# Kernel optimization log

Measured on AMD Instinct MI355X. Metric: run time of the kernel, lower is better.

## Reference

```python
import jax, jax.numpy as jnp
import numpy as np
import math

B, H, L, DK, D, LOCAL = 4, 8, 2048, 64, 512, 4


def setup_inputs() -> dict:
    key = jax.random.key(0)
    ks = jax.random.split(key, 9)
    n = L
    return {
        'query': jax.random.normal(ks[0], (B, H, L, DK), jnp.float32),
        'key': jax.random.normal(ks[1], (B, H, L, DK), jnp.float32),
        'value': jax.random.normal(ks[2], (B, H, L, DK), jnp.float32),
        'users': jax.random.normal(ks[3], (B, L, D), jnp.float32),
        'mask': jnp.tril(jnp.ones((L, L), dtype=bool))[None, None],  # causal [1,1,L,L]
        'rel_pos_w': jax.random.normal(ks[4], (2 * n - 1, DK * LOCAL), jnp.float32) * 0.02,
        'user_proj_w': jax.random.normal(ks[5], (DK * LOCAL, D), jnp.float32) * 0.02,
        'user_proj_b': jax.random.normal(ks[6], (DK * LOCAL,), jnp.float32) * 0.02,
        'mlp_w': jax.random.normal(ks[7], (LOCAL, DK), jnp.float32) * 0.1,
        'mlp_b': jax.random.normal(ks[8], (LOCAL,), jnp.float32) * 0.1,
    }


def reference(query, key, value, users, mask, rel_pos_w, user_proj_w, user_proj_b, mlp_w, mlp_b):
    b, h, l, dk = query.shape
    local = mlp_w.shape[0]
    g = h - local
    n = l
    scale = 1.0 / math.sqrt(dk)
    NEG = -1e12  # MAX_VAL in the torch source

    # ---- global heads: plain softmax attention ----
    qg, kg, vg = query[:, :g], key[:, :g], value[:, :g]
    sg = jnp.einsum('bhqd,bhkd->bhqk', qg, kg) * scale
    sg = jnp.where(mask, sg, NEG)
    pg = jax.nn.softmax(sg, axis=-1)
    og = jnp.einsum('bhqk,bhkd->bhqd', pg, vg)

    # ---- local (LOCKER) heads ----
    ql, kl, vl = query[:, g:], key[:, g:], value[:, g:]
    sl = jnp.einsum('bhqd,bhkd->bhqk', ql, kl) * scale

    # reweight = Linear(d_k,1)(rel_pos + v_q + v_k + user_proj(users)_q) per local head.
    # Linear over a sum decomposes exactly (same math, avoids [b,local,l,l,dk] tensor):
    rel_tab = rel_pos_w.reshape(2 * n - 1, local, dk)
    rel_scores = jnp.einsum('rhd,hd->rh', rel_tab, mlp_w)          # [2n-1, local]
    pos = jnp.arange(n)
    distance = pos[None, :] - pos[:, None] + n - 1                  # [l, l]
    rel_term = rel_scores[distance].transpose(2, 0, 1)              # [local, l, l]

    v_term = jnp.einsum('bhkd,hd->bhk', vl, mlp_w)                  # [b, local, l]
    u = (users @ user_proj_w.T + user_proj_b).reshape(b, l, local, dk)
    u_term = jnp.einsum('bqhd,hd->bhq', u, mlp_w)                   # [b, local, l]

    reweight = (rel_term[None]
                + v_term[:, :, None, :]      # value_l.unsqueeze(-3): varies over key idx
                + v_term[:, :, :, None]      # value_l.unsqueeze(-2): varies over query idx
                + u_term[:, :, :, None]      # user term broadcast over key idx
                + mlp_b[None, :, None, None])

    sl = sl + reweight
    sl = jnp.where(mask, sl, NEG)
    pl = jax.nn.softmax(sl, axis=-1)
    ol = jnp.einsum('bhqk,bhkd->bhqd', pl, vl)

    return jnp.concatenate([og, ol], axis=1)  # [b, h, l, d_k]
```

## Files before the change

kernel.cpp:

```cpp
#include <hip/hip_runtime.h>

#define TL 2048
#define NHEAD 8
#define NLOC 4
#define L2E 1.44269504f
#define PSTRIDE 4352

typedef __attribute__((ext_vector_type(4))) float f32x4;
typedef __attribute__((ext_vector_type(16))) float f32x16;
typedef __attribute__((ext_vector_type(8))) __bf16 bf16x8;
typedef __attribute__((ext_vector_type(8))) unsigned short u16x8;
typedef __attribute__((ext_vector_type(4))) unsigned int u32x4;

static __device__ __forceinline__ unsigned short f2bf(float f) {
    unsigned u = __float_as_uint(f);
    u = (u + 0x7FFFu + ((u >> 16) & 1u)) >> 16;
    return (unsigned short)u;
}
static __device__ __forceinline__ unsigned int cvtpk(float a, float b) {
    unsigned int w;
    asm("v_cvt_pk_bf16_f32 %0, %1, %2" : "=v"(w) : "v"(a), "v"(b));
    return w;
}
static __device__ __forceinline__ void gl_lds16(const void* g, void* l) {
    __builtin_amdgcn_global_load_lds(
        (const __attribute__((address_space(1))) void*)g,
        (__attribute__((address_space(3))) void*)l, 16, 0, 0);
}

__global__ __launch_bounds__(256) void preconv_kernel(
    const float* __restrict__ key, const float* __restrict__ value,
    const float* __restrict__ mlp_w, const float* __restrict__ rel_pos_w,
    unsigned short* __restrict__ Kb, unsigned short* __restrict__ Vtb,
    float* __restrict__ vtbf, float* __restrict__ rel_sf) {
    int blk = blockIdx.x;
    int t = threadIdx.x;
    int wave = t >> 6, lane = t & 63;

    if (blk >= 1024) {
        int r = (blk - 1024) * 4 + wave;
        if (r < 2 * TL - 1) {
#pragma unroll
            for (int hp = 0; hp < 4; ++hp) {
                float v = rel_pos_w[r * 256 + hp * 64 + lane] * mlp_w[hp * 64 + lane];
#pragma unroll
                for (int off = 32; off; off >>= 1) v += __shfl_xor(v, off);
                if (lane == 0) rel_sf[hp * 4096 + r] = v * L2E;
            }
        }
        return;
    }

    __shared__ float Tf[64][66];
    int bh = blk >> 5, kt = blk & 31;
    int h = bh & 7, b = bh >> 3;
    size_t src = (size_t)blk * 4096;
    size_t dst = (size_t)blk * 4096;

    {
        int row = t >> 2, q4 = t & 3;
        const float* kp = key + src + row * 64 + q4 * 16;
#pragma unroll
        for (int j = 0; j < 4; ++j)
            *(f32x4*)&Tf[row][q4 * 16 + j * 4] = *(const f32x4*)(kp + j * 4);
    }
    __syncthreads();
#pragma unroll
    for (int i = 0; i < 2; ++i) {
        int idx = t + i * 256;
        int l31 = idx & 31, hi = (idx >> 5) & 1, mq = (idx >> 6) & 3, h2 = idx >> 8;
        int r = h2 * 32 + l31, c = mq * 2 + hi;
        u16x8 o;
#pragma unroll
        for (int j = 0; j < 8; ++j) o[j] = f2bf(Tf[r][c * 8 + j]);
        *(u16x8*)&Kb[dst + idx * 8] = o;
    }
    __syncthreads();

    {
        int row = t >> 2, q4 = t & 3;
        const float* vp = value + src + row * 64 + q4 * 16;
#pragma unroll
        for (int j = 0; j < 4; ++j)
            *(f32x4*)&Tf[row][q4 * 16 + j * 4] = *(const f32x4*)(vp + j * 4);
    }
    __syncthreads();
#pragma unroll
    for (int i = 0; i < 2; ++i) {
        int idx = t + i * 256;
        int l31 = idx & 31, hi = (idx >> 5) & 1, half = (idx >> 6) & 1, c2 = idx >> 7;
        int r = half * 32 + l31, c = c2 * 2 + hi;
        u16x8 o;
#pragma unroll
        for (int j = 0; j < 8; ++j) o[j] = f2bf(Tf[c * 8 + j][r]);
        *(u16x8*)&Vtb[dst + idx * 8] = o;
    }
    if (h >= NLOC) {
        float mw = mlp_w[(h - NLOC) * 64 + lane];
        float* vout = vtbf + (size_t)((b * NLOC + h - NLOC) * TL) + kt * 64;
#pragma unroll
        for (int i = 0; i < 16; ++i) {
            int row = wave * 16 + i;
            float v = Tf[row][lane] * mw;
#pragma unroll
            for (int off = 32; off; off >>= 1) v += __shfl_xor(v, off);
            if (lane == 0) vout[row] = v * L2E;
        }
    }
}

#define MFMA32(A, B, C) __builtin_amdgcn_mfma_f32_32x32x16_bf16(A, B, C, 0, 0, 0)

__global__ __launch_bounds__(256, 4) void attn_kernel(
    const float* __restrict__ query,
    const unsigned short* __restrict__ Kb, const unsigned short* __restrict__ Vtb,
    const float* __restrict__ rel_sf, const float* __restrict__ vtbf,
    float* __restrict__ part) {

    __shared__ __align__(16) unsigned char smem[35328];
    unsigned short* Ks0 = (unsigned short*)smem;
    unsigned short* Vt0 = (unsigned short*)(smem + 16384);
    float* relw  = (float*)(smem + 32768);
    float* biasf = (float*)(smem + 34816);

    int bid = blockIdx.x;
    int bhx = bid & 31;
    int bh = (bhx & 7) * 4 + (bhx >> 3);
    int sid = bid >> 5;
    int i = 0, s = 0, acc = 0;
    for (int ii = 15; ii >= 0; --ii) {
        int ns = (2 * ii + 7) / 6;
        if (sid >= acc && sid < acc + ns) { i = ii; s = sid - acc; }
        acc += ns;
    }
    int nt = 2 * i + 2;
    int n = (2 * i + 7) / 6;
    int T = nt / n, R = nt % n;
    int k_b = s * T + min(s, R);
    int len = T + (s < R ? 1 : 0);
    int q0 = i << 7;

    int h = bh & 7, b = bh >> 3;
    bool islocal = (h >= NLOC);
    int t = threadIdx.x;
    int w = t >> 6;
    int l31 = t & 31;
    int hi = (t >> 5) & 1;
    int qrel = 32 * w + l31;
    int qglob = q0 + qrel;
    int qmaxw = q0 + 32 * w + 31;
    int hivl = hi * 256 + l31 * 8;

    size_t tbase = (size_t)bh * 32 * 4096;
    const unsigned short* Ktiles = Kb + tbase;
    const unsigned short* Vtiles = Vtb + tbase;
    const float* vtpf = vtbf + (islocal ? (size_t)((b * NLOC + h - NLOC) * TL) : 0);
    int idxlo = 64 * k_b - q0 + 1920;
    const float* relsrc = rel_sf + (islocal ? ((h - NLOC) * 4096 + idxlo) : 0);

    gl_lds16(Ktiles + (size_t)k_b * 4096 + t * 8, Ks0 + t * 8);
    gl_lds16(Ktiles + (size_t)k_b * 4096 + 2048 + t * 8, Ks0 + 2048 + t * 8);
    gl_lds16(Vtiles + (size_t)k_b * 4096 + t * 8, Vt0 + t * 8);
    gl_lds16(Vtiles + (size_t)k_b * 4096 + 2048 + t * 8, Vt0 + 2048 + t * 8);
    if (islocal) {
        if (t < 128) {
            f32x4 v = ((const f32x4*)relsrc)[t];
            ((f32x4*)relw)[t] = v - 20.0f;
        }
        if (t < 16) ((f32x4*)biasf)[t] = ((const f32x4*)(vtpf + (size_t)k_b * 64))[t];
    }

    const float SC = 0.125f * L2E;
    bf16x8 qf[4];
    {
        const float* qsrc = query + ((size_t)bh * TL + qglob) * 64 + 8 * hi;
#pragma unroll
        for (int mq = 0; mq < 4; ++mq) {
            f32x4 a = *(const f32x4*)(qsrc + 16 * mq);
            f32x4 c = *(const f32x4*)(qsrc + 16 * mq + 4);
            u16x8 u;
#pragma unroll
            for (int j = 0; j < 4; ++j) { u[j] = f2bf(a[j] * SC); u[4 + j] = f2bf(c[j] * SC); }
            qf[mq] = __builtin_bit_cast(bf16x8, u);
        }
    }

    float lsum = 0.f;
    f32x16 O0 = {0,0,0,0,0,0,0,0,0,0,0,0,0,0,0,0};
    f32x16 O1 = {0,0,0,0,0,0,0,0,0,0,0,0,0,0,0,0};

    __syncthreads();

    int cur = 0;
#pragma unroll 1
    for (int kt4 = 0; kt4 < len; ++kt4) {
        int kt = k_b + kt4;
        unsigned short* Ks = Ks0 + cur * 4096;
        unsigned short* Vt = Vt0 + cur * 4096;
        const float* bias = biasf + cur * 64;

        if (kt4 + 1 < len) {
            int nb = cur ^ 1;
            const unsigned short* gk = Ktiles + (size_t)(kt + 1) * 4096;
            const unsigned short* gv = Vtiles + (size_t)(kt + 1) * 4096;
            gl_lds16(gk + t * 8, Ks0 + nb * 4096 + t * 8);
            gl_lds16(gk + 2048 + t * 8, Ks0 + nb * 4096 + 2048 + t * 8);
            gl_lds16(gv + t * 8, Vt0 + nb * 4096 + t * 8);
            gl_lds16(gv + 2048 + t * 8, Vt0 + nb * 4096 + 2048 + t * 8);
            if (islocal && t < 16)
                ((f32x4*)(biasf + nb * 64))[t] =
                    ((const f32x4*)(vtpf + (size_t)(kt + 1) * 64))[t];
        }

        bool active = (64 * kt <= qmaxw);
        bool maskt = (64 * kt + 63 > q0 + 32 * w);
        if (active) {
#pragma unroll
            for (int h2 = 0; h2 < 2; ++h2) {
                f32x16 S;
                if (islocal) {
                    int rbase = 64 * kt4 + 32 * h2 + 4 * hi + 127 - qrel;
#pragma unroll
                    for (int g = 0; g < 4; ++g) {
                        f32x4 bv = *(const f32x4*)&bias[32 * h2 + 8 * g + 4 * hi];
#pragma unroll
                        for (int j = 0; j < 4; ++j)
                            S[4 * g + j] = bv[j] + relw[rbase + 8 * g + j];
                    }
                } else {
                    S = (f32x16){-20.f,-20.f,-20.f,-20.f,-20.f,-20.f,-20.f,-20.f,
                                 -20.f,-20.f,-20.f,-20.f,-20.f,-20.f,-20.f,-20.f};
                }
                __builtin_amdgcn_s_setprio(1);
#pragma unroll
                for (int mq = 0; mq < 4; ++mq) {
                    const bf16x8 kf = *(const bf16x8*)&Ks[(h2 * 4 + mq) * 512 + hivl];
                    S = MFMA32(kf, qf[mq], S);
                }
                __builtin_amdgcn_s_setprio(0);

                if (maskt) {
                    int koff = 64 * kt + 32 * h2 + 4 * hi - qglob;
#pragma unroll
                    for (int r = 0; r < 16; ++r) {
                        int kk = (r & 3) + 8 * (r >> 2);
                        if (koff + kk > 0) S[r] = -1e30f;
                    }
                }
                float ps = 0.f;
#pragma unroll
                for (int r = 0; r < 16; ++r) {
                    float p = exp2f(S[r]);
                    S[r] = p; ps += p;
                }
                ps += __shfl_xor(ps, 32);
                lsum += ps;

                __builtin_amdgcn_s_setprio(1);
#pragma unroll
                for (int kq = 0; kq < 2; ++kq) {
                    int ra = 8 * kq;
                    unsigned int x0 = cvtpk(S[ra + 0], S[ra + 1]);
                    unsigned int x1 = cvtpk(S[ra + 2], S[ra + 3]);
                    unsigned int y0 = cvtpk(S[ra + 4], S[ra + 5]);
                    unsigned int y1 = cvtpk(S[ra + 6], S[ra + 7]);
                    asm("v_permlane32_swap_b32 %0, %1" : "+v"(x0), "+v"(y0));
                    asm("v_permlane32_swap_b32 %0, %1" : "+v"(x1), "+v"(y1));
                    u32x4 fw;
                    fw[0] = x0; fw[1] = x1; fw[2] = y0; fw[3] = y1;
                    const bf16x8 pf = __builtin_bit_cast(bf16x8, fw);
                    int c2 = h2 * 2 + kq;
                    const bf16x8 vf0 = *(const bf16x8*)&Vt[c2 * 1024 + hivl];
                    const bf16x8 vf1 = *(const bf16x8*)&Vt[c2 * 1024 + 512 + hivl];
                    O0 = MFMA32(vf0, pf, O0);
                    O1 = MFMA32(vf1, pf, O1);
                }
                __builtin_amdgcn_s_setprio(0);
            }
        }
        __syncthreads();
        cur ^= 1;
    }

    float* pp = part + (size_t)bid * PSTRIDE;
    unsigned int* po = (unsigned int*)pp;
#pragma unroll
    for (int g = 0; g < 4; ++g) {
        unsigned int w0 = cvtpk(O0[4 * g + 0], O0[4 * g + 1]);
        unsigned int w1 = cvtpk(O0[4 * g + 2], O0[4 * g + 3]);
        unsigned int w2 = cvtpk(O1[4 * g + 0], O1[4 * g + 1]);
        unsigned int w3 = cvtpk(O1[4 * g + 2], O1[4 * g + 3]);
        int dp0 = 4 * g + 2 * hi;
        po[dp0 * 128 + qrel] = w0;
        po[(dp0 + 1) * 128 + qrel] = w1;
        po[(16 + dp0) * 128 + qrel] = w2;
        po[(16 + dp0 + 1) * 128 + qrel] = w3;
    }
    if (hi == 0) pp[4096 + qrel] = lsum;
}

__global__ __launch_bounds__(128) void merge_kernel(
    const float* __restrict__ part, float* __restrict__ out) {
    int bid = blockIdx.x;
    int bhx = bid & 31, i = bid >> 5;
    int bh = (bhx & 7) * 4 + (bhx >> 3);
    int n = (2 * i + 7) / 6;
    int sb = 0;
    for (int ii = 15; ii > i; --ii) sb += (2 * ii + 7) / 6;
    int t = threadIdx.x;

    float den = 0.f;
#pragma unroll
    for (int s2 = 0; s2 < 6; ++s2)
        if (s2 < n)
            den += part[(size_t)((sb + s2) * 32 + bhx) * PSTRIDE + 4096 + t];
    float inv = 1.0f / den;

    size_t obase = (size_t)bh * TL * 64 + (size_t)(128 * i + t) * 64;
    for (int seg = 0; seg < 4; ++seg) {
        float o[16];
#pragma unroll
        for (int j = 0; j < 16; ++j) o[j] = 0.f;
#pragma unroll
        for (int s2 = 0; s2 < 6; ++s2) {
            if (s2 < n) {
                const unsigned int* po =
                    (const unsigned int*)(part + (size_t)((sb + s2) * 32 + bhx) * PSTRIDE);
#pragma unroll
                for (int j = 0; j < 8; ++j) {
                    unsigned int wv = po[(seg * 8 + j) * 128 + t];
                    o[2 * j]     += __uint_as_float((wv & 0xffffu) << 16);
                    o[2 * j + 1] += __uint_as_float(wv & 0xffff0000u);
                }
            }
        }
#pragma unroll
        for (int j = 0; j < 16; ++j) o[j] *= inv;
#pragma unroll
        for (int c = 0; c < 4; ++c)
            *(f32x4*)(out + obase + seg * 16 + 4 * c) = *(const f32x4*)&o[4 * c];
    }
}

extern "C" void kernel_launch(void* const* d_in, const int* in_sizes, int n_in,
                              void* d_out, int out_size, void* d_ws, size_t ws_size,
                              hipStream_t stream) {
    const float* query = (const float*)d_in[0];
    const float* key = (const float*)d_in[1];
    const float* value = (const float*)d_in[2];
    const float* rel_pos_w = (const float*)d_in[5];
    const float* mlp_w = (const float*)d_in[8];
    float* out = (float*)d_out;

    unsigned short* Kb = (unsigned short*)d_ws;
    unsigned short* Vtb = Kb + 32 * 32 * 4096;
    float* rel_sf = (float*)(Vtb + 32 * 32 * 4096);
    float* vtbf = rel_sf + 4 * 4096;
    float* part = vtbf + 32768;

    preconv_kernel<<<2048, 256, 0, stream>>>(key, value, mlp_w, rel_pos_w,
                                             Kb, Vtb, vtbf, rel_sf);
    attn_kernel<<<1632, 256, 0, stream>>>(query, Kb, Vtb, rel_sf, vtbf, part);
    merge_kernel<<<512, 128, 0, stream>>>(part, out);
}
```

Measured before the change: 74.40 us.

## Replace LDS double-buffer with register-staged prefetch and single LDS buffer

Drops the direct global-to-LDS double buffer for K/V tiles. The next tile is now prefetched into registers and written into a single LDS buffer after a barrier. This roughly halves shared memory per block, and launch bounds are raised from 4 to 6 blocks per CU to gain occupancy. In exchange it adds a second barrier per iteration and extra registers for the staged data, which could cause spills under the tighter register budget.

New measurement: 134.8 us. 1.81x slower.

```diff
diff --git a/kernel.cpp b/kernel.cpp
--- a/kernel.cpp
+++ b/kernel.cpp
@@ -21,11 +21,6 @@
     unsigned int w;
     asm("v_cvt_pk_bf16_f32 %0, %1, %2" : "=v"(w) : "v"(a), "v"(b));
     return w;
-}
-static __device__ __forceinline__ void gl_lds16(const void* g, void* l) {
-    __builtin_amdgcn_global_load_lds(
-        (const __attribute__((address_space(1))) void*)g,
-        (__attribute__((address_space(3))) void*)l, 16, 0, 0);
 }
 
 __global__ __launch_bounds__(256) void preconv_kernel(
@@ -111,17 +106,17 @@
 
 #define MFMA32(A, B, C) __builtin_amdgcn_mfma_f32_32x32x16_bf16(A, B, C, 0, 0, 0)
 
-__global__ __launch_bounds__(256, 4) void attn_kernel(
+__global__ __launch_bounds__(256, 6) void attn_kernel(
     const float* __restrict__ query,
     const unsigned short* __restrict__ Kb, const unsigned short* __restrict__ Vtb,
     const float* __restrict__ rel_sf, const float* __restrict__ vtbf,
     float* __restrict__ part) {
 
-    __shared__ __align__(16) unsigned char smem[35328];
-    unsigned short* Ks0 = (unsigned short*)smem;
-    unsigned short* Vt0 = (unsigned short*)(smem + 16384);
-    float* relw  = (float*)(smem + 32768);
-    float* biasf = (float*)(smem + 34816);
+    __shared__ __align__(16) unsigned char smem[19456];
+    unsigned short* Ks  = (unsigned short*)smem;
+    unsigned short* Vt  = (unsigned short*)(smem + 8192);
+    float* relw  = (float*)(smem + 16384);
+    float* biasf = (float*)(smem + 18432);
 
     int bid = blockIdx.x;
     int bhx = bid & 31;
@@ -158,10 +153,27 @@
     int idxlo = 64 * k_b - q0 + 1920;
     const float* relsrc = rel_sf + (islocal ? ((h - NLOC) * 4096 + idxlo) : 0);
 
-    gl_lds16(Ktiles + (size_t)k_b * 4096 + t * 8, Ks0 + t * 8);
-    gl_lds16(Ktiles + (size_t)k_b * 4096 + 2048 + t * 8, Ks0 + 2048 + t * 8);
-    gl_lds16(Vtiles + (size_t)k_b * 4096 + t * 8, Vt0 + t * 8);
-    gl_lds16(Vtiles + (size_t)k_b * 4096 + 2048 + t * 8, Vt0 + 2048 + t * 8);
+    u16x8 krA, krB, vrA, vrB;
+    {
+        const unsigned short* gk = Ktiles + (size_t)k_b * 4096;
+        const unsigned short* gv = Vtiles + (size_t)k_b * 4096;
+        krA = *(const u16x8*)(gk + t * 8);
+        krB = *(const u16x8*)(gk + 2048 + t * 8);
+        vrA = *(const u16x8*)(gv + t * 8);
+        vrB = *(const u16x8*)(gv + 2048 + t * 8);
+        *(u16x8*)&Ks[t * 8] = krA;
+        *(u16x8*)&Ks[2048 + t * 8] = krB;
+        *(u16x8*)&Vt[t * 8] = vrA;
+        *(u16x8*)&Vt[2048 + t * 8] = vrB;
+    }
+    if (len > 1) {
+        const unsigned short* gk = Ktiles + (size_t)(k_b + 1) * 4096;
+        const unsigned short* gv = Vtiles + (size_t)(k_b + 1) * 4096;
+        krA = *(const u16x8*)(gk + t * 8);
+        krB = *(const u16x8*)(gk + 2048 + t * 8);
+        vrA = *(const u16x8*)(gv + t * 8);
+        vrB = *(const u16x8*)(gv + 2048 + t * 8);
+    }
     if (islocal) {
         if (t < 128) {
             f32x4 v = ((const f32x4*)relsrc)[t];
@@ -195,22 +207,7 @@
 #pragma unroll 1
     for (int kt4 = 0; kt4 < len; ++kt4) {
         int kt = k_b + kt4;
-        unsigned short* Ks = Ks0 + cur * 4096;
-        unsigned short* Vt = Vt0 + cur * 4096;
         const float* bias = biasf + cur * 64;
-
-        if (kt4 + 1 < len) {
-            int nb = cur ^ 1;
-            const unsigned short* gk = Ktiles + (size_t)(kt + 1) * 4096;
-            const unsigned short* gv = Vtiles + (size_t)(kt + 1) * 4096;
-            gl_lds16(gk + t * 8, Ks0 + nb * 4096 + t * 8);
-            gl_lds16(gk + 2048 + t * 8, Ks0 + nb * 4096 + 2048 + t * 8);
-            gl_lds16(gv + t * 8, Vt0 + nb * 4096 + t * 8);
-            gl_lds16(gv + 2048 + t * 8, Vt0 + nb * 4096 + 2048 + t * 8);
-            if (islocal && t < 16)
-                ((f32x4*)(biasf + nb * 64))[t] =
-                    ((const f32x4*)(vtpf + (size_t)(kt + 1) * 64))[t];
-        }
 
         bool active = (64 * kt <= qmaxw);
         bool maskt = (64 * kt + 63 > q0 + 32 * w);
@@ -279,7 +276,27 @@
             }
         }
         __syncthreads();
-        cur ^= 1;
+
+        if (kt4 + 1 < len) {
+            *(u16x8*)&Ks[t * 8] = krA;
+            *(u16x8*)&Ks[2048 + t * 8] = krB;
+            *(u16x8*)&Vt[t * 8] = vrA;
+            *(u16x8*)&Vt[2048 + t * 8] = vrB;
+            int nb = cur ^ 1;
+            if (islocal && t < 16)
+                ((f32x4*)(biasf + nb * 64))[t] =
+                    ((const f32x4*)(vtpf + (size_t)(kt + 1) * 64))[t];
+            if (kt4 + 2 < len) {
+                const unsigned short* gk = Ktiles + (size_t)(kt + 2) * 4096;
+                const unsigned short* gv = Vtiles + (size_t)(kt + 2) * 4096;
+                krA = *(const u16x8*)(gk + t * 8);
+                krB = *(const u16x8*)(gk + 2048 + t * 8);
+                vrA = *(const u16x8*)(gv + t * 8);
+                vrB = *(const u16x8*)(gv + 2048 + t * 8);
+            }
+            __syncthreads();
+            cur = nb;
+        }
     }
 
     float* pp = part + (size_t)bid * PSTRIDE;
```
